# Kernel tuning notes

Measured on AMD Instinct MI355X. Metric: run time of the kernel, lower is better.

## Reference

```python
import jax, jax.numpy as jnp
import numpy as np

N = 5000
NFEAT = 512
NHID = 64
NHEADS = 8
NCLASS = 40
ALPHA = 0.2  # leaky relu slope
NEG_INF = -9e15


def setup_inputs() -> dict:
    key = jax.random.key(0)
    ks = jax.random.split(key, 12)
    x = jax.random.normal(ks[0], (N, NFEAT), dtype=jnp.float32)
    # binary adjacency, ~32 avg degree, with self loops
    adj = (jax.random.uniform(ks[1], (N, N)) < (32.0 / N)).astype(jnp.float32)
    adj = jnp.maximum(adj, jnp.eye(N, dtype=jnp.float32))
    s = 1.0 / np.sqrt(NFEAT)
    W_h = jax.random.uniform(ks[2], (NHEADS, NFEAT, NHID), minval=-s, maxval=s, dtype=jnp.float32)
    a_h = jax.random.uniform(ks[3], (NHEADS, 2 * NHID), minval=-s, maxval=s, dtype=jnp.float32)
    s2 = 1.0 / np.sqrt(NHID * NHEADS)
    W_o = jax.random.uniform(ks[4], (NHID * NHEADS, NHID), minval=-s2, maxval=s2, dtype=jnp.float32)
    a_o = jax.random.uniform(ks[5], (2 * NHID,), minval=-s2, maxval=s2, dtype=jnp.float32)
    s3 = 1.0 / np.sqrt(NHID)
    fc1_w = jax.random.uniform(ks[6], (NHID, 200), minval=-s3, maxval=s3, dtype=jnp.float32)
    fc1_b = jax.random.uniform(ks[7], (200,), minval=-s3, maxval=s3, dtype=jnp.float32)
    s4 = 1.0 / np.sqrt(200)
    fc2_w = jax.random.uniform(ks[8], (200, NCLASS), minval=-s4, maxval=s4, dtype=jnp.float32)
    fc2_b = jax.random.uniform(ks[9], (NCLASS,), minval=-s4, maxval=s4, dtype=jnp.float32)
    return {"x": x, "adj": adj, "W_h": W_h, "a_h": a_h, "W_o": W_o, "a_o": a_o,
            "fc1_w": fc1_w, "fc1_b": fc1_b, "fc2_w": fc2_w, "fc2_b": fc2_b}


def _masked_attention(e, adj):
    # e: [..., N, N]; mask where adj == 0, then row softmax
    e = jnp.where(adj > 0, e, NEG_INF)
    return jax.nn.softmax(e, axis=-1)


def reference(x, adj, W_h, a_h, W_o, a_o, fc1_w, fc1_b, fc2_w, fc2_b):
    # ---- multi-head GAT layer (concat=True), eval mode (dropout off) ----
    Wh = jnp.einsum('nf,hfo->hno', x, W_h)                 # [H, N, nhid]
    f1 = jnp.einsum('hno,ho->hn', Wh, a_h[:, :NHID])       # [H, N]
    f2 = jnp.einsum('hno,ho->hn', Wh, a_h[:, NHID:])       # [H, N]
    e = jax.nn.leaky_relu(f1[:, :, None] + f2[:, None, :], ALPHA)  # [H, N, N]
    att = _masked_attention(e, adj[None, :, :])
    h = jnp.einsum('hnm,hmo->hno', att, Wh)                # [H, N, nhid]
    h1 = jax.nn.elu(h).transpose(1, 0, 2).reshape(N, NHEADS * NHID)  # concat heads

    # ---- output GAT layer (concat=False) ----
    Wh2 = h1 @ W_o                                         # [N, nhid]
    g1 = Wh2 @ a_o[:NHID]                                  # [N]
    g2 = Wh2 @ a_o[NHID:]                                  # [N]
    e2 = jax.nn.leaky_relu(g1[:, None] + g2[None, :], ALPHA)
    att2 = _masked_attention(e2, adj)
    h2 = att2 @ Wh2                                        # [N, nhid]

    # ---- MLP head ----
    h3 = jax.nn.elu(h2 @ fc1_w + fc1_b)
    return h3 @ fc2_w + fc2_b                              # [N, nclass]
```

## Files before the change

### kernel.cpp

```cpp
#include <hip/hip_runtime.h>

typedef unsigned short u16;
typedef unsigned int u32;
typedef __bf16 bf16_t;
typedef __bf16 bf16x8 __attribute__((ext_vector_type(8)));
typedef float f32x4 __attribute__((ext_vector_type(4)));

#define NN 5000
#define NF 512
#define NH 64
#define HEADS 8
#define NCLS 40
#define CAP 128
#define LRELU 0.2f

__device__ __forceinline__ bool adj_is_bf16(const void* adj) {
    return ((*(const u32*)adj) & 0xFFFFu) != 0u;
}
__device__ __forceinline__ u16 rne_bf16(float f) {
    u32 u = __float_as_uint(f);
    u += 0x7FFFu + ((u >> 16) & 1u);
    return (u16)(u >> 16);
}
__device__ __forceinline__ float up_bf16(u16 h) {
    return __uint_as_float((u32)h << 16);
}

__global__ __launch_bounds__(256) void cvt_ab(const void* __restrict__ x,
                                              const void* __restrict__ W_h,
                                              const void* __restrict__ adj,
                                              u16* __restrict__ xc, u16* __restrict__ whc) {
    const bool isb = adj_is_bf16(adj);
    const int total = NN * NF + HEADS * NF * NH;
    for (int i = blockIdx.x * 256 + threadIdx.x; i < total; i += gridDim.x * 256) {
        const void* src; u16* dst; int off;
        if (i < NN * NF) { src = x; dst = xc; off = i; }
        else             { src = W_h; dst = whc; off = i - NN * NF; }
        dst[off] = isb ? ((const u16*)src)[off] : rne_bf16(((const float*)src)[off]);
    }
}

__global__ __launch_bounds__(256) void cvt_small(const void* a_h, const void* W_o, const void* a_o,
                                                 const void* f1w, const void* f1b,
                                                 const void* f2w, const void* f2b,
                                                 const void* adj,
                                                 float* a_hc, float* W_oc, float* a_oc,
                                                 float* f1wc, float* f1bc, float* f2wc, float* f2bc) {
    const bool isb = adj_is_bf16(adj);
    const int s0 = HEADS * 2 * NH, s1 = HEADS * NH * NH, s2 = 2 * NH,
              s3 = NH * 200, s4 = 200, s5 = 200 * NCLS, s6 = NCLS;
    const int total = s0 + s1 + s2 + s3 + s4 + s5 + s6;
    for (int i = blockIdx.x * 256 + threadIdx.x; i < total; i += gridDim.x * 256) {
        const void* src; float* dst; int off = i;
        if (off < s0) { src = a_h; dst = a_hc; }
        else if ((off -= s0) < s1) { src = W_o;  dst = W_oc; }
        else if ((off -= s1) < s2) { src = a_o;  dst = a_oc; }
        else if ((off -= s2) < s3) { src = f1w;  dst = f1wc; }
        else if ((off -= s3) < s4) { src = f1b;  dst = f1bc; }
        else if ((off -= s4) < s5) { src = f2w;  dst = f2wc; }
        else { off -= s5;           src = f2b;  dst = f2bc; }
        dst[off] = isb ? up_bf16(((const u16*)src)[off]) : ((const float*)src)[off];
    }
}

__global__ __launch_bounds__(256) void build_csr(const void* __restrict__ adj,
                                                 int* __restrict__ nbr,
                                                 int* __restrict__ deg) {
    const int n = blockIdx.x;
    const bool isb = adj_is_bf16(adj);
    __shared__ int cnt;
    if (threadIdx.x == 0) cnt = 0;
    __syncthreads();
    int* nrow = nbr + (size_t)n * CAP;
    if (isb) {
        const uint4* row4 = (const uint4*)((const u16*)adj + (size_t)n * NN);
        for (int c = threadIdx.x; c < NN / 8; c += 256) {
            uint4 v = row4[c];
            u32 w[4] = {v.x, v.y, v.z, v.w};
            int base = c * 8;
            #pragma unroll
            for (int q = 0; q < 4; ++q) {
                if (w[q] & 0xFFFFu) { int p = atomicAdd(&cnt, 1); if (p < CAP) nrow[p] = base + 2 * q; }
                if (w[q] >> 16)     { int p = atomicAdd(&cnt, 1); if (p < CAP) nrow[p] = base + 2 * q + 1; }
            }
        }
    } else {
        const uint4* row4 = (const uint4*)((const float*)adj + (size_t)n * NN);
        for (int c = threadIdx.x; c < NN / 4; c += 256) {
            uint4 v = row4[c];
            u32 w[4] = {v.x, v.y, v.z, v.w};
            int base = c * 4;
            #pragma unroll
            for (int q = 0; q < 4; ++q)
                if (w[q]) { int p = atomicAdd(&cnt, 1); if (p < CAP) nrow[p] = base + q; }
        }
    }
    __syncthreads();
    if (threadIdx.x == 0) deg[n] = cnt < CAP ? cnt : CAP;
}

__global__ __launch_bounds__(256) void gemm1_mfma(const bf16_t* __restrict__ x,
                                                  const bf16_t* __restrict__ W_h,
                                                  float* __restrict__ Wh) {
    const int lane = threadIdx.x & 63;
    const int wid  = threadIdx.x >> 6;
    const int rg = blockIdx.x;
    const int ct = blockIdx.y;
    const int h  = blockIdx.z;
    const int quad = lane >> 4;
    const int lr   = lane & 15;
    const int kq   = quad * 8;
    const int nCol = ct * 16 + lr;
    const bf16_t* Bh = W_h + (size_t)h * NF * NH;

    bf16x8 bfrag[16];
    #pragma unroll
    for (int s = 0; s < 16; ++s) {
        bf16x8 b;
        #pragma unroll
        for (int j = 0; j < 8; ++j) b[j] = Bh[(s * 32 + kq + j) * NH + nCol];
        bfrag[s] = b;
    }

    for (int rt = rg * 4 + wid; rt < (NN + 15) / 16; rt += 80) {
        int row  = rt * 16 + lr;
        int rowc = row < NN ? row : NN - 1;
        const bf16_t* xp = x + (size_t)rowc * NF + kq;
        f32x4 acc = {0.f, 0.f, 0.f, 0.f};
        #pragma unroll
        for (int s = 0; s < 16; ++s) {
            bf16x8 a = *(const bf16x8*)(xp + s * 32);
            acc = __builtin_amdgcn_mfma_f32_16x16x32_bf16(a, bfrag[s], acc, 0, 0, 0);
        }
        #pragma unroll
        for (int r = 0; r < 4; ++r) {
            int gr = rt * 16 + quad * 4 + r;
            if (gr < NN) Wh[((size_t)(h * NN + gr)) * NH + ct * 16 + lr] = acc[r];
        }
    }
}

__global__ __launch_bounds__(256) void attn_coef(const float* __restrict__ Wh,
                                                 const float* __restrict__ a_h,
                                                 float* __restrict__ f1,
                                                 float* __restrict__ f2) {
    const int lane = threadIdx.x & 63;
    const int gw = blockIdx.x * 4 + (threadIdx.x >> 6);
    const int h = gw / NN;
    float w  = Wh[(size_t)gw * NH + lane];
    float p1 = w * a_h[h * 128 + lane];
    float p2 = w * a_h[h * 128 + NH + lane];
    #pragma unroll
    for (int o = 32; o; o >>= 1) { p1 += __shfl_xor(p1, o); p2 += __shfl_xor(p2, o); }
    if (lane == 0) { f1[gw] = p1; f2[gw] = p2; }
}

__global__ __launch_bounds__(256) void agg1(const float* __restrict__ Wh,
                                            const float* __restrict__ f1,
                                            const float* __restrict__ f2,
                                            const int* __restrict__ nbr,
                                            const int* __restrict__ deg,
                                            float* __restrict__ h1) {
    const int lane = threadIdx.x & 63;
    const int wid  = threadIdx.x >> 6;
    const int gw = blockIdx.x * 4 + wid;
    const int h = gw / NN;
    const int n = gw - h * NN;
    __shared__ float s_alpha[4][CAP];
    __shared__ int   s_nbr[4][CAP];
    const int d = deg[n];
    const int* nb = nbr + (size_t)n * CAP;
    const float f1n = f1[gw];
    const float* f2h = f2 + (size_t)h * NN;

    float mx = -INFINITY;
    for (int j = lane; j < d; j += 64) {
        int m = nb[j];
        s_nbr[wid][j] = m;
        float e = f1n + f2h[m];
        e = e > 0.f ? e : LRELU * e;
        s_alpha[wid][j] = e;
        mx = fmaxf(mx, e);
    }
    #pragma unroll
    for (int o = 32; o; o >>= 1) mx = fmaxf(mx, __shfl_xor(mx, o));
    float sm = 0.f;
    for (int j = lane; j < d; j += 64) {
        float p = expf(s_alpha[wid][j] - mx);
        s_alpha[wid][j] = p;
        sm += p;
    }
    #pragma unroll
    for (int o = 32; o; o >>= 1) sm += __shfl_xor(sm, o);
    __syncthreads();

    float acc = 0.f;
    const float* WhH = Wh + (size_t)h * NN * NH;
    for (int j = 0; j < d; ++j)
        acc += s_alpha[wid][j] * WhH[(size_t)s_nbr[wid][j] * NH + lane];
    float hv = acc / sm;
    hv = hv > 0.f ? hv : expf(hv) - 1.f;
    h1[(size_t)n * (HEADS * NH) + h * NH + lane] = hv;
}

__global__ __launch_bounds__(256) void gemm2(const float* __restrict__ h1,
                                             const float* __restrict__ W_o,
                                             const float* __restrict__ a_o,
                                             float* __restrict__ Wh2,
                                             float* __restrict__ g1,
                                             float* __restrict__ g2) {
    const int lane = threadIdx.x & 63;
    const int wid  = threadIdx.x >> 6;
    const int n = blockIdx.x * 4 + wid;
    __shared__ float sh[4][HEADS * NH];
    const float4* hr = (const float4*)(h1 + (size_t)n * (HEADS * NH));
    ((float4*)sh[wid])[lane]      = hr[lane];
    ((float4*)sh[wid])[lane + 64] = hr[lane + 64];
    __syncthreads();
    float acc = 0.f;
    #pragma unroll 8
    for (int f = 0; f < HEADS * NH; ++f)
        acc += sh[wid][f] * W_o[f * NH + lane];
    Wh2[(size_t)n * NH + lane] = acc;
    float p1 = acc * a_o[lane];
    float p2 = acc * a_o[NH + lane];
    #pragma unroll
    for (int o = 32; o; o >>= 1) { p1 += __shfl_xor(p1, o); p2 += __shfl_xor(p2, o); }
    if (lane == 0) { g1[n] = p1; g2[n] = p2; }
}

__global__ __launch_bounds__(256) void agg2_mlp(const float* __restrict__ Wh2,
                                                const float* __restrict__ g1,
                                                const float* __restrict__ g2,
                                                const int* __restrict__ nbr,
                                                const int* __restrict__ deg,
                                                const float* __restrict__ fc1_w,
                                                const float* __restrict__ fc1_b,
                                                const float* __restrict__ fc2_w,
                                                const float* __restrict__ fc2_b,
                                                float* __restrict__ out) {
    const int lane = threadIdx.x & 63;
    const int wid  = threadIdx.x >> 6;
    const int n = blockIdx.x * 4 + wid;
    __shared__ float s_alpha[4][CAP];
    __shared__ int   s_nbr[4][CAP];
    __shared__ float s_h2[4][NH];
    __shared__ float s_h3[4][200];
    const int d = deg[n];
    const int* nb = nbr + (size_t)n * CAP;
    const float gn = g1[n];

    float mx = -INFINITY;
    for (int j = lane; j < d; j += 64) {
        int m = nb[j];
        s_nbr[wid][j] = m;
        float e = gn + g2[m];
        e = e > 0.f ? e : LRELU * e;
        s_alpha[wid][j] = e;
        mx = fmaxf(mx, e);
    }
    #pragma unroll
    for (int o = 32; o; o >>= 1) mx = fmaxf(mx, __shfl_xor(mx, o));
    float sm = 0.f;
    for (int j = lane; j < d; j += 64) {
        float p = expf(s_alpha[wid][j] - mx);
        s_alpha[wid][j] = p;
        sm += p;
    }
    #pragma unroll
    for (int o = 32; o; o >>= 1) sm += __shfl_xor(sm, o);
    __syncthreads();

    float acc = 0.f;
    for (int j = 0; j < d; ++j)
        acc += s_alpha[wid][j] * Wh2[(size_t)s_nbr[wid][j] * NH + lane];
    s_h2[wid][lane] = acc / sm;
    __syncthreads();

    for (int o = lane; o < 200; o += 64) {
        float a = fc1_b[o];
        #pragma unroll 8
        for (int f = 0; f < NH; ++f) a += s_h2[wid][f] * fc1_w[f * 200 + o];
        s_h3[wid][o] = a > 0.f ? a : expf(a) - 1.f;
    }
    __syncthreads();

    if (lane < NCLS) {
        float a = fc2_b[lane];
        #pragma unroll 8
        for (int f = 0; f < 200; ++f) a += s_h3[wid][f] * fc2_w[f * NCLS + lane];
        out[(size_t)n * NCLS + lane] = a;
    }
}

extern "C" void kernel_launch(void* const* d_in, const int* in_sizes, int n_in,
                              void* d_out, int out_size, void* d_ws, size_t ws_size,
                              hipStream_t stream) {
    const void* x     = d_in[0];
    const void* adj   = d_in[1];
    const void* W_h   = d_in[2];
    const void* a_h   = d_in[3];
    const void* W_o   = d_in[4];
    const void* a_o   = d_in[5];
    const void* fc1_w = d_in[6];
    const void* fc1_b = d_in[7];
    const void* fc2_w = d_in[8];
    const void* fc2_b = d_in[9];
    float* out = (float*)d_out;

    char* ws = (char*)d_ws;
    int*   nbr   = (int*)(ws + 0);
    int*   deg   = (int*)(ws + 2560000);
    float* Wh    = (float*)(ws + 2580000);
    float* f1    = (float*)(ws + 12820000);
    float* f2    = (float*)(ws + 12980000);
    float* h1    = (float*)(ws + 13140000);
    float* Wh2   = (float*)(ws + 23380000);
    float* g1    = (float*)(ws + 24660000);
    float* g2    = (float*)(ws + 24680000);
    u16*   xc    = (u16*)(ws + 24700000);
    u16*   whc   = (u16*)(ws + 29820000);
    float* a_hc  = (float*)(ws + 30344288);
    float* W_oc  = (float*)(ws + 30348384);
    float* a_oc  = (float*)(ws + 30479456);
    float* f1wc  = (float*)(ws + 30479968);
    float* f1bc  = (float*)(ws + 30531168);
    float* f2wc  = (float*)(ws + 30531968);
    float* f2bc  = (float*)(ws + 30563968);

    cvt_ab<<<2048, 256, 0, stream>>>(x, W_h, adj, xc, whc);
    cvt_small<<<64, 256, 0, stream>>>(a_h, W_o, a_o, fc1_w, fc1_b, fc2_w, fc2_b, adj,
                                      a_hc, W_oc, a_oc, f1wc, f1bc, f2wc, f2bc);
    build_csr<<<NN, 256, 0, stream>>>(adj, nbr, deg);
    gemm1_mfma<<<dim3(20, 4, HEADS), 256, 0, stream>>>((const bf16_t*)xc, (const bf16_t*)whc, Wh);
    attn_coef<<<HEADS * NN / 4, 256, 0, stream>>>(Wh, a_hc, f1, f2);
    agg1<<<HEADS * NN / 4, 256, 0, stream>>>(Wh, f1, f2, nbr, deg, h1);
    gemm2<<<NN / 4, 256, 0, stream>>>(h1, W_oc, a_oc, Wh2, g1, g2);
    agg2_mlp<<<NN / 4, 256, 0, stream>>>(Wh2, g1, g2, nbr, deg,
                                         f1wc, f1bc, f2wc, f2bc, out);
}
```

Baseline: 295.8 us.

## Fuse prep kernels, fold attention coefs into GEMM1, batch rows in GEMM2 and MLP

The three preprocessing kernels (convert x/W_h, convert small weights, build CSR) become one launch with block ranges. The attention-coefficient projection moves into the MFMA GEMM epilogue, so the separate attn_coef kernel is dropped. GEMM1 is regridded so each wave owns a 16-column slice. GEMM2 and the MLP head now process four nodes per block and reuse each weight load across them, and the neighbour aggregation loops use two accumulators. This cuts launches and weight-traffic redundancy, at the cost of more shared memory and block-level syncs. It also removes a __syncthreads before aggregation in agg1.

```diff
diff --git a/kernel.cpp b/kernel.cpp
--- a/kernel.cpp
+++ b/kernel.cpp
@@ -26,104 +26,105 @@
     return __uint_as_float((u32)h << 16);
 }
 
-__global__ __launch_bounds__(256) void cvt_ab(const void* __restrict__ x,
-                                              const void* __restrict__ W_h,
-                                              const void* __restrict__ adj,
-                                              u16* __restrict__ xc, u16* __restrict__ whc) {
+#define CVT_AB_BLKS 344
+__global__ __launch_bounds__(256) void prep(const void* __restrict__ x, const void* __restrict__ W_h,
+                                            const void* __restrict__ adj,
+                                            const void* a_h, const void* W_o, const void* a_o,
+                                            const void* f1w, const void* f1b,
+                                            const void* f2w, const void* f2b,
+                                            u16* __restrict__ xc, u16* __restrict__ whc,
+                                            float* a_hc, float* W_oc, float* a_oc,
+                                            float* f1wc, float* f1bc, float* f2wc, float* f2bc,
+                                            int* __restrict__ nbr, int* __restrict__ deg) {
     const bool isb = adj_is_bf16(adj);
-    const int total = NN * NF + HEADS * NF * NH;
-    for (int i = blockIdx.x * 256 + threadIdx.x; i < total; i += gridDim.x * 256) {
-        const void* src; u16* dst; int off;
-        if (i < NN * NF) { src = x; dst = xc; off = i; }
-        else             { src = W_h; dst = whc; off = i - NN * NF; }
-        dst[off] = isb ? ((const u16*)src)[off] : rne_bf16(((const float*)src)[off]);
-    }
-}
-
-__global__ __launch_bounds__(256) void cvt_small(const void* a_h, const void* W_o, const void* a_o,
-                                                 const void* f1w, const void* f1b,
-                                                 const void* f2w, const void* f2b,
-                                                 const void* adj,
-                                                 float* a_hc, float* W_oc, float* a_oc,
-                                                 float* f1wc, float* f1bc, float* f2wc, float* f2bc) {
-    const bool isb = adj_is_bf16(adj);
-    const int s0 = HEADS * 2 * NH, s1 = HEADS * NH * NH, s2 = 2 * NH,
-              s3 = NH * 200, s4 = 200, s5 = 200 * NCLS, s6 = NCLS;
-    const int total = s0 + s1 + s2 + s3 + s4 + s5 + s6;
-    for (int i = blockIdx.x * 256 + threadIdx.x; i < total; i += gridDim.x * 256) {
-        const void* src; float* dst; int off = i;
-        if (off < s0) { src = a_h; dst = a_hc; }
-        else if ((off -= s0) < s1) { src = W_o;  dst = W_oc; }
-        else if ((off -= s1) < s2) { src = a_o;  dst = a_oc; }
-        else if ((off -= s2) < s3) { src = f1w;  dst = f1wc; }
-        else if ((off -= s3) < s4) { src = f1b;  dst = f1bc; }
-        else if ((off -= s4) < s5) { src = f2w;  dst = f2wc; }
-        else { off -= s5;           src = f2b;  dst = f2bc; }
-        dst[off] = isb ? up_bf16(((const u16*)src)[off]) : ((const float*)src)[off];
-    }
-}
-
-__global__ __launch_bounds__(256) void build_csr(const void* __restrict__ adj,
-                                                 int* __restrict__ nbr,
-                                                 int* __restrict__ deg) {
-    const int n = blockIdx.x;
-    const bool isb = adj_is_bf16(adj);
-    __shared__ int cnt;
-    if (threadIdx.x == 0) cnt = 0;
-    __syncthreads();
-    int* nrow = nbr + (size_t)n * CAP;
-    if (isb) {
-        const uint4* row4 = (const uint4*)((const u16*)adj + (size_t)n * NN);
-        for (int c = threadIdx.x; c < NN / 8; c += 256) {
-            uint4 v = row4[c];
-            u32 w[4] = {v.x, v.y, v.z, v.w};
-            int base = c * 8;
-            #pragma unroll
-            for (int q = 0; q < 4; ++q) {
-                if (w[q] & 0xFFFFu) { int p = atomicAdd(&cnt, 1); if (p < CAP) nrow[p] = base + 2 * q; }
-                if (w[q] >> 16)     { int p = atomicAdd(&cnt, 1); if (p < CAP) nrow[p] = base + 2 * q + 1; }
+    const int b = blockIdx.x;
+    if (b < NN) {
+        __shared__ int cnt;
+        if (threadIdx.x == 0) cnt = 0;
+        __syncthreads();
+        int* nrow = nbr + (size_t)b * CAP;
+        if (isb) {
+            const uint4* row4 = (const uint4*)((const u16*)adj + (size_t)b * NN);
+            for (int c = threadIdx.x; c < NN / 8; c += 256) {
+                uint4 v = row4[c];
+                u32 w[4] = {v.x, v.y, v.z, v.w};
+                int base = c * 8;
+                #pragma unroll
+                for (int q = 0; q < 4; ++q) {
+                    if (w[q] & 0xFFFFu) { int p = atomicAdd(&cnt, 1); if (p < CAP) nrow[p] = base + 2 * q; }
+                    if (w[q] >> 16)     { int p = atomicAdd(&cnt, 1); if (p < CAP) nrow[p] = base + 2 * q + 1; }
+                }
             }
+        } else {
+            const uint4* row4 = (const uint4*)((const float*)adj + (size_t)b * NN);
+            for (int c = threadIdx.x; c < NN / 4; c += 256) {
+                uint4 v = row4[c];
+                u32 w[4] = {v.x, v.y, v.z, v.w};
+                int base = c * 4;
+                #pragma unroll
+                for (int q = 0; q < 4; ++q)
+                    if (w[q]) { int p = atomicAdd(&cnt, 1); if (p < CAP) nrow[p] = base + q; }
+            }
+        }
+        __syncthreads();
+        if (threadIdx.x == 0) deg[b] = cnt < CAP ? cnt : CAP;
+    } else if (b < NN + CVT_AB_BLKS) {
+        const int total = NN * NF + HEADS * NF * NH;
+        for (int i = (b - NN) * 256 + threadIdx.x; i < total; i += CVT_AB_BLKS * 256) {
+            const void* src; u16* dst; int off;
+            if (i < NN * NF) { src = x; dst = xc; off = i; }
+            else             { src = W_h; dst = whc; off = i - NN * NF; }
+            dst[off] = isb ? ((const u16*)src)[off] : rne_bf16(((const float*)src)[off]);
         }
     } else {
-        const uint4* row4 = (const uint4*)((const float*)adj + (size_t)n * NN);
-        for (int c = threadIdx.x; c < NN / 4; c += 256) {
-            uint4 v = row4[c];
-            u32 w[4] = {v.x, v.y, v.z, v.w};
-            int base = c * 4;
-            #pragma unroll
-            for (int q = 0; q < 4; ++q)
-                if (w[q]) { int p = atomicAdd(&cnt, 1); if (p < CAP) nrow[p] = base + q; }
-        }
-    }
-    __syncthreads();
-    if (threadIdx.x == 0) deg[n] = cnt < CAP ? cnt : CAP;
-}
-
-__global__ __launch_bounds__(256) void gemm1_mfma(const bf16_t* __restrict__ x,
-                                                  const bf16_t* __restrict__ W_h,
-                                                  float* __restrict__ Wh) {
+        const int s0 = HEADS * 2 * NH, s1 = HEADS * NH * NH, s2 = 2 * NH,
+                  s3 = NH * 200, s4 = 200, s5 = 200 * NCLS, s6 = NCLS;
+        const int total = s0 + s1 + s2 + s3 + s4 + s5 + s6;
+        for (int i = (b - NN - CVT_AB_BLKS) * 256 + threadIdx.x; i < total; i += 8 * 256) {
+            const void* src; float* dst; int off = i;
+            if (off < s0) { src = a_h; dst = a_hc; }
+            else if ((off -= s0) < s1) { src = W_o;  dst = W_oc; }
+            else if ((off -= s1) < s2) { src = a_o;  dst = a_oc; }
+            else if ((off -= s2) < s3) { src = f1w;  dst = f1wc; }
+            else if ((off -= s3) < s4) { src = f1b;  dst = f1bc; }
+            else if ((off -= s4) < s5) { src = f2w;  dst = f2wc; }
+            else { off -= s5;           src = f2b;  dst = f2bc; }
+            dst[off] = isb ? up_bf16(((const u16*)src)[off]) : ((const float*)src)[off];
+        }
+    }
+}
+
+__global__ __launch_bounds__(256) void gemm1_f(const bf16_t* __restrict__ x,
+                                               const bf16_t* __restrict__ W_h,
+                                               const float* __restrict__ a_h,
+                                               float* __restrict__ Wh,
+                                               float* __restrict__ f1,
+                                               float* __restrict__ f2) {
     const int lane = threadIdx.x & 63;
     const int wid  = threadIdx.x >> 6;
     const int rg = blockIdx.x;
-    const int ct = blockIdx.y;
-    const int h  = blockIdx.z;
+    const int h  = blockIdx.y;
     const int quad = lane >> 4;
     const int lr   = lane & 15;
     const int kq   = quad * 8;
-    const int nCol = ct * 16 + lr;
+    const int nCol = wid * 16 + lr;
     const bf16_t* Bh = W_h + (size_t)h * NF * NH;
+    __shared__ float f1s[4][64], f2s[4][64];
 
     bf16x8 bfrag[16];
     #pragma unroll
     for (int s = 0; s < 16; ++s) {
-        bf16x8 b;
+        bf16x8 bb;
         #pragma unroll
-        for (int j = 0; j < 8; ++j) b[j] = Bh[(s * 32 + kq + j) * NH + nCol];
-        bfrag[s] = b;
-    }
-
-    for (int rt = rg * 4 + wid; rt < (NN + 15) / 16; rt += 80) {
-        int row  = rt * 16 + lr;
+        for (int j = 0; j < 8; ++j) bb[j] = Bh[(s * 32 + kq + j) * NH + nCol];
+        bfrag[s] = bb;
+    }
+    const float a1c = a_h[h * 128 + nCol];
+    const float a2c = a_h[h * 128 + NH + nCol];
+
+    for (int t = 0; t < 4; ++t) {
+        const int rb = rg * 64 + t * 16;
+        int row  = rb + lr;
         int rowc = row < NN ? row : NN - 1;
         const bf16_t* xp = x + (size_t)rowc * NF + kq;
         f32x4 acc = {0.f, 0.f, 0.f, 0.f};
@@ -134,25 +135,22 @@
         }
         #pragma unroll
         for (int r = 0; r < 4; ++r) {
-            int gr = rt * 16 + quad * 4 + r;
-            if (gr < NN) Wh[((size_t)(h * NN + gr)) * NH + ct * 16 + lr] = acc[r];
-        }
-    }
-}
-
-__global__ __launch_bounds__(256) void attn_coef(const float* __restrict__ Wh,
-                                                 const float* __restrict__ a_h,
-                                                 float* __restrict__ f1,
-                                                 float* __restrict__ f2) {
-    const int lane = threadIdx.x & 63;
-    const int gw = blockIdx.x * 4 + (threadIdx.x >> 6);
-    const int h = gw / NN;
-    float w  = Wh[(size_t)gw * NH + lane];
-    float p1 = w * a_h[h * 128 + lane];
-    float p2 = w * a_h[h * 128 + NH + lane];
-    #pragma unroll
-    for (int o = 32; o; o >>= 1) { p1 += __shfl_xor(p1, o); p2 += __shfl_xor(p2, o); }
-    if (lane == 0) { f1[gw] = p1; f2[gw] = p2; }
+            int gr = rb + quad * 4 + r;
+            if (gr < NN) Wh[((size_t)(h * NN + gr)) * NH + nCol] = acc[r];
+            float p1 = acc[r] * a1c, p2 = acc[r] * a2c;
+            #pragma unroll
+            for (int o = 8; o; o >>= 1) { p1 += __shfl_xor(p1, o); p2 += __shfl_xor(p2, o); }
+            if (lr == 0) { f1s[wid][t * 16 + quad * 4 + r] = p1; f2s[wid][t * 16 + quad * 4 + r] = p2; }
+        }
+    }
+    __syncthreads();
+    if (wid == 0) {
+        int gr = rg * 64 + lane;
+        if (gr < NN) {
+            f1[h * NN + gr] = f1s[0][lane] + f1s[1][lane] + f1s[2][lane] + f1s[3][lane];
+            f2[h * NN + gr] = f2s[0][lane] + f2s[1][lane] + f2s[2][lane] + f2s[3][lane];
+        }
+    }
 }
 
 __global__ __launch_bounds__(256) void agg1(const float* __restrict__ Wh,
@@ -192,41 +190,52 @@
     }
     #pragma unroll
     for (int o = 32; o; o >>= 1) sm += __shfl_xor(sm, o);
-    __syncthreads();
-
-    float acc = 0.f;
-    const float* WhH = Wh + (size_t)h * NN * NH;
-    for (int j = 0; j < d; ++j)
-        acc += s_alpha[wid][j] * WhH[(size_t)s_nbr[wid][j] * NH + lane];
-    float hv = acc / sm;
+
+    float acc0 = 0.f, acc1 = 0.f;
+    const float* WhL = Wh + (size_t)h * NN * NH + lane;
+    int j = 0;
+    for (; j + 2 <= d; j += 2) {
+        acc0 += s_alpha[wid][j]     * WhL[(size_t)s_nbr[wid][j]     * NH];
+        acc1 += s_alpha[wid][j + 1] * WhL[(size_t)s_nbr[wid][j + 1] * NH];
+    }
+    if (j < d) acc0 += s_alpha[wid][j] * WhL[(size_t)s_nbr[wid][j] * NH];
+    float hv = (acc0 + acc1) / sm;
     hv = hv > 0.f ? hv : expf(hv) - 1.f;
     h1[(size_t)n * (HEADS * NH) + h * NH + lane] = hv;
 }
 
-__global__ __launch_bounds__(256) void gemm2(const float* __restrict__ h1,
-                                             const float* __restrict__ W_o,
-                                             const float* __restrict__ a_o,
-                                             float* __restrict__ Wh2,
-                                             float* __restrict__ g1,
-                                             float* __restrict__ g2) {
-    const int lane = threadIdx.x & 63;
-    const int wid  = threadIdx.x >> 6;
-    const int n = blockIdx.x * 4 + wid;
-    __shared__ float sh[4][HEADS * NH];
-    const float4* hr = (const float4*)(h1 + (size_t)n * (HEADS * NH));
-    ((float4*)sh[wid])[lane]      = hr[lane];
-    ((float4*)sh[wid])[lane + 64] = hr[lane + 64];
-    __syncthreads();
-    float acc = 0.f;
-    #pragma unroll 8
-    for (int f = 0; f < HEADS * NH; ++f)
-        acc += sh[wid][f] * W_o[f * NH + lane];
-    Wh2[(size_t)n * NH + lane] = acc;
-    float p1 = acc * a_o[lane];
-    float p2 = acc * a_o[NH + lane];
-    #pragma unroll
-    for (int o = 32; o; o >>= 1) { p1 += __shfl_xor(p1, o); p2 += __shfl_xor(p2, o); }
-    if (lane == 0) { g1[n] = p1; g2[n] = p2; }
+__global__ __launch_bounds__(256) void gemm2_4(const float* __restrict__ h1,
+                                               const float* __restrict__ W_o,
+                                               const float* __restrict__ a_o,
+                                               float* __restrict__ Wh2,
+                                               float* __restrict__ g1,
+                                               float* __restrict__ g2) {
+    const int t = threadIdx.x;
+    const int n0 = blockIdx.x * 4;
+    __shared__ float sh[4 * 512];
+    __shared__ float ps[4][4][64];
+    const float4* src = (const float4*)(h1 + (size_t)n0 * 512);
+    ((float4*)sh)[t]       = src[t];
+    ((float4*)sh)[t + 256] = src[t + 256];
+    __syncthreads();
+    const int o = t & 63, part = t >> 6;
+    float a0 = 0.f, a1 = 0.f, a2 = 0.f, a3 = 0.f;
+    const float* wo = W_o + part * 128 * 64 + o;
+    const float* s0 = sh + part * 128;
+    #pragma unroll 4
+    for (int f = 0; f < 128; ++f) {
+        float w = wo[f * 64];
+        a0 += s0[f] * w; a1 += s0[512 + f] * w; a2 += s0[1024 + f] * w; a3 += s0[1536 + f] * w;
+    }
+    ps[part][0][o] = a0; ps[part][1][o] = a1; ps[part][2][o] = a2; ps[part][3][o] = a3;
+    __syncthreads();
+    const int nd = t >> 6;
+    float w2 = ps[0][nd][o] + ps[1][nd][o] + ps[2][nd][o] + ps[3][nd][o];
+    Wh2[(size_t)(n0 + nd) * 64 + o] = w2;
+    float p1 = w2 * a_o[o], p2 = w2 * a_o[64 + o];
+    #pragma unroll
+    for (int s = 32; s; s >>= 1) { p1 += __shfl_xor(p1, s); p2 += __shfl_xor(p2, s); }
+    if (o == 0) { g1[n0 + nd] = p1; g2[n0 + nd] = p2; }
 }
 
 __global__ __launch_bounds__(256) void agg2_mlp(const float* __restrict__ Wh2,
@@ -241,11 +250,14 @@
                                                 float* __restrict__ out) {
     const int lane = threadIdx.x & 63;
     const int wid  = threadIdx.x >> 6;
-    const int n = blockIdx.x * 4 + wid;
+    const int t = threadIdx.x;
+    const int n0 = blockIdx.x * 4;
+    const int n = n0 + wid;
     __shared__ float s_alpha[4][CAP];
     __shared__ int   s_nbr[4][CAP];
     __shared__ float s_h2[4][NH];
     __shared__ float s_h3[4][200];
+    __shared__ float ps2[2][4][NCLS];
     const int d = deg[n];
     const int* nb = nbr + (size_t)n * CAP;
     const float gn = g1[n];
@@ -269,27 +281,47 @@
     }
     #pragma unroll
     for (int o = 32; o; o >>= 1) sm += __shfl_xor(sm, o);
-    __syncthreads();
-
-    float acc = 0.f;
-    for (int j = 0; j < d; ++j)
-        acc += s_alpha[wid][j] * Wh2[(size_t)s_nbr[wid][j] * NH + lane];
-    s_h2[wid][lane] = acc / sm;
-    __syncthreads();
-
-    for (int o = lane; o < 200; o += 64) {
-        float a = fc1_b[o];
-        #pragma unroll 8
-        for (int f = 0; f < NH; ++f) a += s_h2[wid][f] * fc1_w[f * 200 + o];
-        s_h3[wid][o] = a > 0.f ? a : expf(a) - 1.f;
-    }
-    __syncthreads();
-
-    if (lane < NCLS) {
-        float a = fc2_b[lane];
-        #pragma unroll 8
-        for (int f = 0; f < 200; ++f) a += s_h3[wid][f] * fc2_w[f * NCLS + lane];
-        out[(size_t)n * NCLS + lane] = a;
+
+    float acc0 = 0.f, acc1 = 0.f;
+    int j = 0;
+    for (; j + 2 <= d; j += 2) {
+        acc0 += s_alpha[wid][j]     * Wh2[(size_t)s_nbr[wid][j]     * NH + lane];
+        acc1 += s_alpha[wid][j + 1] * Wh2[(size_t)s_nbr[wid][j + 1] * NH + lane];
+    }
+    if (j < d) acc0 += s_alpha[wid][j] * Wh2[(size_t)s_nbr[wid][j] * NH + lane];
+    s_h2[wid][lane] = (acc0 + acc1) / sm;
+    __syncthreads();
+
+    if (t < 200) {
+        float b0 = 0.f, b1 = 0.f, b2 = 0.f, b3 = 0.f;
+        #pragma unroll 4
+        for (int f = 0; f < NH; ++f) {
+            float w = fc1_w[f * 200 + t];
+            b0 += s_h2[0][f] * w; b1 += s_h2[1][f] * w; b2 += s_h2[2][f] * w; b3 += s_h2[3][f] * w;
+        }
+        float bb = fc1_b[t];
+        b0 += bb; b1 += bb; b2 += bb; b3 += bb;
+        s_h3[0][t] = b0 > 0.f ? b0 : expf(b0) - 1.f;
+        s_h3[1][t] = b1 > 0.f ? b1 : expf(b1) - 1.f;
+        s_h3[2][t] = b2 > 0.f ? b2 : expf(b2) - 1.f;
+        s_h3[3][t] = b3 > 0.f ? b3 : expf(b3) - 1.f;
+    }
+    __syncthreads();
+
+    if (t < 80) {
+        const int o = t % 40, fh = t / 40;
+        float c0 = 0.f, c1 = 0.f, c2 = 0.f, c3 = 0.f;
+        #pragma unroll 4
+        for (int f = fh * 100; f < fh * 100 + 100; ++f) {
+            float w = fc2_w[f * NCLS + o];
+            c0 += s_h3[0][f] * w; c1 += s_h3[1][f] * w; c2 += s_h3[2][f] * w; c3 += s_h3[3][f] * w;
+        }
+        ps2[fh][0][o] = c0; ps2[fh][1][o] = c1; ps2[fh][2][o] = c2; ps2[fh][3][o] = c3;
+    }
+    __syncthreads();
+    if (t < 160) {
+        const int nd = t / 40, o = t % 40;
+        out[(size_t)(n0 + nd) * NCLS + o] = ps2[0][nd][o] + ps2[1][nd][o] + fc2_b[o];
     }
 }
 
@@ -328,14 +360,14 @@
     float* f2wc  = (float*)(ws + 30531968);
     float* f2bc  = (float*)(ws + 30563968);
 
-    cvt_ab<<<2048, 256, 0, stream>>>(x, W_h, adj, xc, whc);
-    cvt_small<<<64, 256, 0, stream>>>(a_h, W_o, a_o, fc1_w, fc1_b, fc2_w, fc2_b, adj,
-                                      a_hc, W_oc, a_oc, f1wc, f1bc, f2wc, f2bc);
-    build_csr<<<NN, 256, 0, stream>>>(adj, nbr, deg);
-    gemm1_mfma<<<dim3(20, 4, HEADS), 256, 0, stream>>>((const bf16_t*)xc, (const bf16_t*)whc, Wh);
-    attn_coef<<<HEADS * NN / 4, 256, 0, stream>>>(Wh, a_hc, f1, f2);
+    prep<<<NN + CVT_AB_BLKS + 8, 256, 0, stream>>>(x, W_h, adj, a_h, W_o, a_o,
+                                                   fc1_w, fc1_b, fc2_w, fc2_b,
+                                                   xc, whc, a_hc, W_oc, a_oc,
+                                                   f1wc, f1bc, f2wc, f2bc, nbr, deg);
+    gemm1_f<<<dim3(79, HEADS), 256, 0, stream>>>((const bf16_t*)xc, (const bf16_t*)whc,
+                                                 a_hc, Wh, f1, f2);
     agg1<<<HEADS * NN / 4, 256, 0, stream>>>(Wh, f1, f2, nbr, deg, h1);
-    gemm2<<<NN / 4, 256, 0, stream>>>(h1, W_oc, a_oc, Wh2, g1, g2);
+    gemm2_4<<<NN / 4, 256, 0, stream>>>(h1, W_oc, a_oc, Wh2, g1, g2);
     agg2_mlp<<<NN / 4, 256, 0, stream>>>(Wh2, g1, g2, nbr, deg,
                                          f1wc, f1bc, f2wc, f2bc, out);
 }
```

Result: faster. 281.9 us (-4.7%).
